# Kernel tuning notes

Hardware: AMD Instinct MI355X
Metric: run time of the kernel (lower is better)

The kernel has to match this reference:

```python
import jax, jax.numpy as jnp
import numpy as np
from functools import reduce

IN_CH = 1; OUT_CH = 16; K = 3; PAD = 1; QDEPTH = 2; WIRES = 4; DIM = 2 ** WIRES

# --- precomputed CNOT permutation matrices (constants) ---
# PennyLane convention: wire 0 is the most significant bit of the basis index.
def _cnot_mat(control, target):
    perm = np.arange(DIM)
    cbit = 1 << (WIRES - 1 - control)
    tbit = 1 << (WIRES - 1 - target)
    flip = (perm & cbit).astype(bool)
    perm = np.where(flip, perm ^ tbit, perm)
    return jnp.asarray(np.eye(DIM, dtype=np.complex64)[perm])

# StronglyEntanglingLayers default ranges: r_l = l % (n_wires - 1) + 1
_CNOTS = [[_cnot_mat(i, (i + (l % (WIRES - 1) + 1)) % WIRES) for i in range(WIRES)]
          for l in range(QDEPTH)]

def _rot(angles):
    # qml.Rot(phi, theta, omega) = RZ(omega) @ RY(theta) @ RZ(phi)
    phi, theta, omega = angles[0], angles[1], angles[2]
    c = jnp.cos(theta / 2); s = jnp.sin(theta / 2)
    return jnp.stack([
        jnp.exp(-0.5j * (phi + omega)) * c, -jnp.exp(0.5j * (phi - omega)) * s,
        jnp.exp(-0.5j * (phi - omega)) * s,  jnp.exp(0.5j * (phi + omega)) * c,
    ]).reshape(2, 2)

def _sel_unitary(weights):
    # Full 16x16 unitary of StronglyEntanglingLayers(weights) -- dim is tiny,
    # so building the dense unitary once and batching patches through it is
    # the efficient form (vs. per-gate contractions over 2.1M state vectors).
    U = jnp.eye(DIM, dtype=jnp.complex64)
    for l in range(QDEPTH):
        layer = reduce(jnp.kron, [_rot(weights[l, i]) for i in range(WIRES)])
        U = layer @ U
        for C in _CNOTS[l]:
            U = C @ U
    return U

def setup_inputs() -> dict:
    key = jax.random.key(0)
    k1, k2 = jax.random.split(key)
    x = jax.random.normal(k1, (32, 1, 256, 256), dtype=jnp.float32)
    weights = jax.random.uniform(k2, (QDEPTH, WIRES, 3), dtype=jnp.float32)
    return {"x": x, "weights": weights}

def reference(x, weights):
    b, c, h_in, w_in = x.shape
    h_out = h_in + 2 * PAD - K + 1
    w_out = w_in + 2 * PAD - K + 1
    # ConstantPad2d with value 0.01
    xp = jnp.pad(x, ((0, 0), (0, 0), (PAD, PAD), (PAD, PAD)), constant_values=0.01)
    # unfold -> (b, c*K*K, h_out, w_out), feature order (c, k0, k1)
    patches = jax.lax.conv_general_dilated_patches(xp, (K, K), (1, 1), 'VALID')
    patches = patches.transpose(0, 2, 3, 1).reshape(b * h_out * w_out, K * K)
    # zero-pad patch vectors from K*K=9 to 2^wires=16, then L2-normalize (eps=1e-12)
    patches = jnp.pad(patches, ((0, 0), (0, DIM - K * K)))
    norm = jnp.linalg.norm(patches, axis=-1, keepdims=True)
    patches = patches / jnp.maximum(norm, 1e-12)
    # Mottonen prep on |0> yields the normalized patch exactly (up to global
    # phase); then apply the entangling-layer unitary and measure probs.
    state = patches.astype(jnp.complex64) @ _sel_unitary(weights).T  # (N, 16)
    probs = jnp.abs(state) ** 2
    out = jnp.clip(probs * (DIM * 0.5), 0.0, 1.0)[:, :OUT_CH]
    return out.reshape(b, h_out, w_out, OUT_CH).transpose(0, 3, 1, 2)
```

## Files before the change

kernel.cpp:

```cpp
#include <hip/hip_runtime.h>
#include <math.h>


#define WIRES 4
#define DIM 16

__device__ inline void rot_entry(float phi, float th, float om, int rb, int cb,
                                 float& er, float& ei) {
    float a = 0.5f * (phi + om);
    float b = 0.5f * (phi - om);
    float cc = cosf(0.5f * th), ss = sinf(0.5f * th);
    if (rb == 0 && cb == 0) { er = cc * cosf(a); ei = -cc * sinf(a); }
    else if (rb == 0 && cb == 1) { er = -ss * cosf(b); ei = -ss * sinf(b); }
    else if (rb == 1 && cb == 0) { er = ss * cosf(b); ei = -ss * sinf(b); }
    else { er = cc * cosf(a); ei = cc * sinf(a); }
}

__device__ inline void layer_elem(const float* __restrict__ w, int l, int r,
                                  int c, float& pr, float& pi) {
    pr = 1.f; pi = 0.f;
    #pragma unroll
    for (int i = 0; i < WIRES; ++i) {
        const float* wi = w + (l * WIRES + i) * 3;
        float er, ei;
        int rb = (r >> (3 - i)) & 1, cb = (c >> (3 - i)) & 1;
        rot_entry(wi[0], wi[1], wi[2], rb, cb, er, ei);
        float nr = pr * er - pi * ei;
        float ni = pr * ei + pi * er;
        pr = nr; pi = ni;
    }
}

__device__ inline int cnot_src(int r, int range) {
    int src = r;
    #pragma unroll
    for (int i = WIRES - 1; i >= 0; --i) {
        int control = i, target = (i + range) & 3;
        int cbit = 1 << (3 - control), tbit = 1 << (3 - target);
        if (src & cbit) src ^= tbit;
    }
    return src;
}

__global__ __launch_bounds__(256) void build_unitary(
        const float* __restrict__ w, float* __restrict__ uout) {
    __shared__ float Lr[DIM][DIM], Li[DIM][DIM];
    __shared__ float Ur[DIM][DIM], Ui[DIM][DIM];
    __shared__ float Tr[DIM][DIM], Ti[DIM][DIM];
    int t = threadIdx.x;
    int r = t >> 4, c = t & 15;

    float lr, li;
    layer_elem(w, 0, r, c, lr, li);
    Lr[r][c] = lr; Li[r][c] = li;
    __syncthreads();
    int s0 = cnot_src(r, 1);
    Ur[r][c] = Lr[s0][c]; Ui[r][c] = Li[s0][c];
    __syncthreads();

    layer_elem(w, 1, r, c, lr, li);
    Lr[r][c] = lr; Li[r][c] = li;
    __syncthreads();
    float ar = 0.f, ai = 0.f;
    #pragma unroll
    for (int m = 0; m < DIM; ++m) {
        float xr = Lr[r][m], xi = Li[r][m];
        float yr = Ur[m][c], yi = Ui[m][c];
        ar += xr * yr - xi * yi;
        ai += xr * yi + xi * yr;
    }
    Tr[r][c] = ar; Ti[r][c] = ai;
    __syncthreads();
    int s1 = cnot_src(r, 2);
    uout[r * DIM + c]           = Tr[s1][c];
    uout[256 + r * DIM + c]     = Ti[s1][c];
}

#define H 256
#define W 256
#define NB 32
#define OUTC 16

__global__ __launch_bounds__(256) void qconv_kernel(
        const float* __restrict__ x, const float* __restrict__ u,
        float* __restrict__ out) {
    __shared__ float sUr[OUTC][9];
    __shared__ float sUi[OUTC][9];
    __shared__ float rows[3][W + 8];

    int t = threadIdx.x;
    int blk = blockIdx.x;
    int i = blk & (H - 1);
    int b = blk >> 8;

    if (t < OUTC * 9) {
        int k = t / 9, m = t % 9;
        sUr[k][m] = u[k * DIM + m];
        sUi[k][m] = u[256 + k * DIM + m];
    }

    const float* xb = x + (size_t)b * H * W;
    #pragma unroll
    for (int di = 0; di < 3; ++di) {
        int row = i + di - 1;
        for (int cpos = t; cpos < W + 2; cpos += 256) {
            int j = cpos - 1;
            float v = 0.01f;
            if ((unsigned)row < (unsigned)H && (unsigned)j < (unsigned)W)
                v = xb[row * W + j];
            rows[di][cpos] = v;
        }
    }
    __syncthreads();

    float p[9];
    #pragma unroll
    for (int di = 0; di < 3; ++di)
        #pragma unroll
        for (int dj = 0; dj < 3; ++dj)
            p[di * 3 + dj] = rows[di][t + dj];

    float n2 = 0.f;
    #pragma unroll
    for (int m = 0; m < 9; ++m) n2 = fmaf(p[m], p[m], n2);
    float factor = 8.0f / fmaxf(n2, 1e-24f);

    float* ob = out + (size_t)b * OUTC * H * W + (size_t)i * W + t;
    #pragma unroll
    for (int k = 0; k < OUTC; ++k) {
        float sr = 0.f, si = 0.f;
        #pragma unroll
        for (int m = 0; m < 9; ++m) {
            sr = fmaf(sUr[k][m], p[m], sr);
            si = fmaf(sUi[k][m], p[m], si);
        }
        float v = factor * (sr * sr + si * si);
        ob[(size_t)k * H * W] = fminf(v, 1.0f);
    }
}

extern "C" void kernel_launch(void* const* d_in, const int* in_sizes, int n_in,
                              void* d_out, int out_size, void* d_ws, size_t ws_size,
                              hipStream_t stream) {
    const float* x = (const float*)d_in[0];
    const float* w = (const float*)d_in[1];
    float* out = (float*)d_out;
    float* uws = (float*)d_ws;

    build_unitary<<<1, 256, 0, stream>>>(w, uws);
    qconv_kernel<<<NB * H, 256, 0, stream>>>(x, uws, out);
}
```

Measured before the change: 172.8 us.

## Process 4 rows and 4 pixels per thread with vectorized loads and stores

Each block now handles four output rows with a six-row halo tile in shared memory. Each thread computes four adjacent pixels from a register sliding window and writes float4 outputs. The unitary is repacked as interleaved real/imag pairs so coefficients load as vectors. This cuts block count, redundant halo loads and scalar store instructions, at the cost of more registers per thread.

```diff
diff --git a/kernel.cpp b/kernel.cpp
--- a/kernel.cpp
+++ b/kernel.cpp
@@ -72,70 +72,110 @@
     Tr[r][c] = ar; Ti[r][c] = ai;
     __syncthreads();
     int s1 = cnot_src(r, 2);
-    uout[r * DIM + c]           = Tr[s1][c];
-    uout[256 + r * DIM + c]     = Ti[s1][c];
+    if (c < 9) {
+        uout[r * 20 + 2 * c]     = Tr[s1][c];
+        uout[r * 20 + 2 * c + 1] = Ti[s1][c];
+    }
 }
 
 #define H 256
 #define W 256
 #define NB 32
 #define OUTC 16
+#define RPB 4
 
 __global__ __launch_bounds__(256) void qconv_kernel(
         const float* __restrict__ x, const float* __restrict__ u,
         float* __restrict__ out) {
-    __shared__ float sUr[OUTC][9];
-    __shared__ float sUi[OUTC][9];
-    __shared__ float rows[3][W + 8];
+    __shared__ float sU[OUTC][20];
+    __shared__ float rows[RPB + 2][W + 8];
 
     int t = threadIdx.x;
     int blk = blockIdx.x;
-    int i = blk & (H - 1);
-    int b = blk >> 8;
+    int b = blk >> 6;
+    int i0 = (blk & 63) << 2;
 
-    if (t < OUTC * 9) {
-        int k = t / 9, m = t % 9;
-        sUr[k][m] = u[k * DIM + m];
-        sUi[k][m] = u[256 + k * DIM + m];
+    {
+        float* sUf = &sU[0][0];
+        sUf[t & 255] = u[t & 255];
+        if (t < 64) sUf[t + 256] = u[t + 256];
     }
 
-    const float* xb = x + (size_t)b * H * W;
+    const float* xb = x + (size_t)b * (H * W);
     #pragma unroll
-    for (int di = 0; di < 3; ++di) {
-        int row = i + di - 1;
+    for (int wr = 0; wr < RPB + 2; ++wr) {
+        int row = i0 + wr - 1;
+        bool rok = (unsigned)row < (unsigned)H;
         for (int cpos = t; cpos < W + 2; cpos += 256) {
             int j = cpos - 1;
             float v = 0.01f;
-            if ((unsigned)row < (unsigned)H && (unsigned)j < (unsigned)W)
-                v = xb[row * W + j];
-            rows[di][cpos] = v;
+            if (rok && (unsigned)j < (unsigned)W) v = xb[row * W + j];
+            rows[wr][cpos] = v;
         }
     }
     __syncthreads();
 
-    float p[9];
+    int rl = t >> 6;
+    int c  = (t & 63) << 2;
+    int i  = i0 + rl;
+
+    float win[3][6];
     #pragma unroll
-    for (int di = 0; di < 3; ++di)
+    for (int di = 0; di < 3; ++di) {
+        float4 a = *(const float4*)&rows[rl + di][c];
+        float4 bq = *(const float4*)&rows[rl + di][c + 4];
+        win[di][0] = a.x;  win[di][1] = a.y;  win[di][2] = a.z;
+        win[di][3] = a.w;  win[di][4] = bq.x; win[di][5] = bq.y;
+    }
+
+    float fac[4];
+    #pragma unroll
+    for (int px = 0; px < 4; ++px) {
+        float n2 = 0.f;
         #pragma unroll
-        for (int dj = 0; dj < 3; ++dj)
-            p[di * 3 + dj] = rows[di][t + dj];
+        for (int di = 0; di < 3; ++di)
+            #pragma unroll
+            for (int dj = 0; dj < 3; ++dj) {
+                float pv = win[di][px + dj];
+                n2 = fmaf(pv, pv, n2);
+            }
+        fac[px] = 8.0f / fmaxf(n2, 1e-24f);
+    }
 
-    float n2 = 0.f;
-    #pragma unroll
-    for (int m = 0; m < 9; ++m) n2 = fmaf(p[m], p[m], n2);
-    float factor = 8.0f / fmaxf(n2, 1e-24f);
-
-    float* ob = out + (size_t)b * OUTC * H * W + (size_t)i * W + t;
+    float* ob = out + (size_t)b * OUTC * (H * W) + (size_t)i * W + c;
     #pragma unroll
     for (int k = 0; k < OUTC; ++k) {
-        float sr = 0.f, si = 0.f;
+        float4 q0 = *(const float4*)&sU[k][0];
+        float4 q1 = *(const float4*)&sU[k][4];
+        float4 q2 = *(const float4*)&sU[k][8];
+        float4 q3 = *(const float4*)&sU[k][12];
+        float2 q4 = *(const float2*)&sU[k][16];
+        float4 res;
         #pragma unroll
-        for (int m = 0; m < 9; ++m) {
-            sr = fmaf(sUr[k][m], p[m], sr);
-            si = fmaf(sUi[k][m], p[m], si);
+        for (int px = 0; px < 4; ++px) {
+            float sr, si;
+            sr = q0.x * win[0][px];
+            si = q0.y * win[0][px];
+            sr = fmaf(q0.z, win[0][px + 1], sr);
+            si = fmaf(q0.w, win[0][px + 1], si);
+            sr = fmaf(q1.x, win[0][px + 2], sr);
+            si = fmaf(q1.y, win[0][px + 2], si);
+            sr = fmaf(q1.z, win[1][px], sr);
+            si = fmaf(q1.w, win[1][px], si);
+            sr = fmaf(q2.x, win[1][px + 1], sr);
+            si = fmaf(q2.y, win[1][px + 1], si);
+            sr = fmaf(q2.z, win[1][px + 2], sr);
+            si = fmaf(q2.w, win[1][px + 2], si);
+            sr = fmaf(q3.x, win[2][px], sr);
+            si = fmaf(q3.y, win[2][px], si);
+            sr = fmaf(q3.z, win[2][px + 1], sr);
+            si = fmaf(q3.w, win[2][px + 1], si);
+            sr = fmaf(q4.x, win[2][px + 2], sr);
+            si = fmaf(q4.y, win[2][px + 2], si);
+            float v = fac[px] * fmaf(sr, sr, si * si);
+            ((float*)&res)[px] = fminf(v, 1.0f);
         }
-        float v = factor * (sr * sr + si * si);
-        ob[(size_t)k * H * W] = fminf(v, 1.0f);
+        *(float4*)&ob[(size_t)k * (H * W)] = res;
     }
 }
 
@@ -148,5 +188,5 @@
     float* uws = (float*)d_ws;
 
     build_unitary<<<1, 256, 0, stream>>>(w, uws);
-    qconv_kernel<<<NB * H, 256, 0, stream>>>(x, uws, out);
+    qconv_kernel<<<NB * H / RPB, 256, 0, stream>>>(x, uws, out);
 }
```

Measured after the change: 163.8 us. 5.2% less time.
